# Kernel tuning notes

Hardware: AMD Instinct MI355X
Metric: run time of the kernel (lower is better)

Reference implementation:

```python
import jax, jax.numpy as jnp
import numpy as np

ND_WEIGHT = 1.0
NUM_CLASS = 1000
B, D = 16384, 2048


def setup_inputs() -> dict:
    key = jax.random.key(0)
    k1, k2, k3, k4 = jax.random.split(key, 4)
    s_emb = jax.random.normal(k1, (B, D), dtype=jnp.float32)
    t_emb = jax.random.normal(k2, (B, D), dtype=jnp.float32)
    T_EMB = jax.random.normal(k3, (NUM_CLASS, D), dtype=jnp.float32)
    labels = jax.random.randint(k4, (B,), 0, NUM_CLASS, dtype=jnp.int64)
    return {"s_emb": s_emb, "t_emb": t_emb, "T_EMB": T_EMB, "labels": labels}


def reference(s_emb, t_emb, T_EMB, labels):
    # Gather per-sample class centers: [B, D]
    centers = T_EMB[labels]
    # Unit-normalize each center (L2 along feature dim)
    e_c = centers / jnp.linalg.norm(centers, axis=-1, keepdims=True)
    # Per-sample max of student/teacher embedding norms: [B]
    s_norm = jnp.linalg.norm(s_emb, axis=-1)
    t_norm = jnp.linalg.norm(t_emb, axis=-1)
    max_norm = jnp.maximum(s_norm, t_norm)
    # 1 - <s, e_c> / max_norm, summed then averaged, scaled by nd_weight
    dots = jnp.sum(s_emb * e_c, axis=-1)
    loss_sum = jnp.sum(1.0 - dots / max_norm)
    return loss_sum * ND_WEIGHT / s_emb.shape[0]
```

## Files before the change

### kernel.cpp

```cpp
#include <hip/hip_runtime.h>


#define NROWS  16384
#define DDIM   2048
#define BLK    256
#define WPB    (BLK / 64)
#define RPW    4
#define GRID   (NROWS / (WPB * RPW))
#define GRID_AT (NROWS / WPB)

typedef float v4f __attribute__((ext_vector_type(4)));

__device__ __forceinline__ float dot4(const v4f a, const v4f b) {
    return a.x*b.x + a.y*b.y + a.z*b.z + a.w*b.w;
}

__global__ __launch_bounds__(BLK, 1) void dnl_main_kernel(
    const float* __restrict__ s_emb,
    const float* __restrict__ t_emb,
    const float* __restrict__ T_EMB,
    const int*   __restrict__ labels,
    float*       __restrict__ partial)
{
    const int tid  = threadIdx.x;
    const int lane = tid & 63;
    const int wave = blockIdx.x * WPB + (tid >> 6);
    const int row0 = wave * RPW;

    v4f sA[8], tA[8], cA[8];
    v4f sB[8], tB[8], cB[8];

    auto issue = [&](int row, v4f* S, v4f* T, v4f* C) {
        const int label = labels[row];
        const v4f* s4 = (const v4f*)(s_emb + (size_t)row   * DDIM);
        const v4f* t4 = (const v4f*)(t_emb + (size_t)row   * DDIM);
        const v4f* c4 = (const v4f*)(T_EMB + (size_t)label * DDIM);
        #pragma unroll
        for (int j = 0; j < 8; ++j) {
            const int k = lane + j * 64;
            S[j] = s4[k];
            T[j] = t4[k];
            C[j] = c4[k];
        }
    };

    auto consume = [&](int row, const v4f* S, const v4f* T, const v4f* C) {
        float ss = 0.f, tt = 0.f, sc = 0.f, cc = 0.f;
        #pragma unroll
        for (int j = 0; j < 8; ++j) {
            ss += dot4(S[j], S[j]);
            tt += dot4(T[j], T[j]);
            sc += dot4(S[j], C[j]);
            cc += dot4(C[j], C[j]);
        }
        #pragma unroll
        for (int off = 32; off > 0; off >>= 1) {
            ss += __shfl_xor(ss, off, 64);
            tt += __shfl_xor(tt, off, 64);
            sc += __shfl_xor(sc, off, 64);
            cc += __shfl_xor(cc, off, 64);
        }
        if (lane == 0) {
            const float max_norm = fmaxf(sqrtf(ss), sqrtf(tt));
            partial[row] = 1.0f - sc / (sqrtf(cc) * max_norm);
        }
    };

    issue  (row0 + 0, sA, tA, cA);
    issue  (row0 + 1, sB, tB, cB);
    consume(row0 + 0, sA, tA, cA);
    issue  (row0 + 2, sA, tA, cA);
    consume(row0 + 1, sB, tB, cB);
    issue  (row0 + 3, sB, tB, cB);
    consume(row0 + 2, sA, tA, cA);
    consume(row0 + 3, sB, tB, cB);
}

__global__ __launch_bounds__(BLK) void dnl_reduce_kernel(
    const float* __restrict__ partial,
    float*       __restrict__ out)
{
    const int tid = threadIdx.x;
    const float4* p4 = (const float4*)partial;
    float sum = 0.f;
    #pragma unroll
    for (int j = 0; j < 16; ++j) {
        const float4 v = p4[tid + j * BLK];
        sum += v.x + v.y + v.z + v.w;
    }

    #pragma unroll
    for (int off = 32; off > 0; off >>= 1)
        sum += __shfl_xor(sum, off, 64);

    __shared__ float red[4];
    if ((tid & 63) == 0) red[tid >> 6] = sum;
    __syncthreads();
    if (tid == 0)
        out[0] = (red[0] + red[1] + red[2] + red[3]) * (1.0f / (float)NROWS);
}

__global__ __launch_bounds__(BLK, 2) void dnl_main_atomic_kernel(
    const float* __restrict__ s_emb,
    const float* __restrict__ t_emb,
    const float* __restrict__ T_EMB,
    const int*   __restrict__ labels,
    float*       __restrict__ out)
{
    const int tid  = threadIdx.x;
    const int lane = tid & 63;
    const int row  = blockIdx.x * WPB + (tid >> 6);
    const int label = labels[row];

    const v4f* s4 = (const v4f*)(s_emb + (size_t)row   * DDIM);
    const v4f* t4 = (const v4f*)(t_emb + (size_t)row   * DDIM);
    const v4f* c4 = (const v4f*)(T_EMB + (size_t)label * DDIM);

    float ss = 0.f, tt = 0.f, sc = 0.f, cc = 0.f;
    #pragma unroll
    for (int j = 0; j < 8; ++j) {
        const int k = lane + j * 64;
        const v4f s = s4[k];
        const v4f t = t4[k];
        const v4f c = c4[k];
        ss += dot4(s, s);
        tt += dot4(t, t);
        sc += dot4(s, c);
        cc += dot4(c, c);
    }
    #pragma unroll
    for (int off = 32; off > 0; off >>= 1) {
        ss += __shfl_xor(ss, off, 64);
        tt += __shfl_xor(tt, off, 64);
        sc += __shfl_xor(sc, off, 64);
        cc += __shfl_xor(cc, off, 64);
    }
    if (lane == 0) {
        const float max_norm = fmaxf(sqrtf(ss), sqrtf(tt));
        atomicAdd(out, (1.0f - sc / (sqrtf(cc) * max_norm)) * (1.0f / (float)NROWS));
    }
}

extern "C" void kernel_launch(void* const* d_in, const int* in_sizes, int n_in,
                              void* d_out, int out_size, void* d_ws, size_t ws_size,
                              hipStream_t stream) {
    const float* s_emb  = (const float*)d_in[0];
    const float* t_emb  = (const float*)d_in[1];
    const float* T_EMB  = (const float*)d_in[2];
    const int*   labels = (const int*)d_in[3];
    float* out = (float*)d_out;

    if (ws_size >= (size_t)NROWS * sizeof(float)) {
        float* partial = (float*)d_ws;
        dnl_main_kernel<<<GRID, BLK, 0, stream>>>(s_emb, t_emb, T_EMB, labels, partial);
        dnl_reduce_kernel<<<1, BLK, 0, stream>>>(partial, out);
    } else {
        hipMemsetAsync(d_out, 0, sizeof(float), stream);
        dnl_main_atomic_kernel<<<GRID_AT, BLK, 0, stream>>>(s_emb, t_emb, T_EMB, labels, out);
    }
}
```

Measured before the change: 281.8 us.

## Bucket rows by label so each block reuses one class center from LDS

Adds a single-block histogram/scan kernel that groups row indices by label, then launches one block per class. Each block loads its center into LDS once, computes its norm once, and streams only the s and t rows for that class. This removes redundant center reads and per-row center-norm work. In exchange it adds a serial one-block sort kernel, an extra launch, load imbalance across classes, and one wave per row without the previous explicit load pipelining.

Result: slower. 306.3 us (+8.7%).

```diff
diff --git a/kernel.cpp b/kernel.cpp
--- a/kernel.cpp
+++ b/kernel.cpp
@@ -3,10 +3,9 @@
 
 #define NROWS  16384
 #define DDIM   2048
+#define NLAB   1000
 #define BLK    256
 #define WPB    (BLK / 64)
-#define RPW    4
-#define GRID   (NROWS / (WPB * RPW))
 #define GRID_AT (NROWS / WPB)
 
 typedef float v4f __attribute__((ext_vector_type(4)));
@@ -15,65 +14,106 @@
     return a.x*b.x + a.y*b.y + a.z*b.z + a.w*b.w;
 }
 
-__global__ __launch_bounds__(BLK, 1) void dnl_main_kernel(
+__global__ __launch_bounds__(1024) void dnl_hist_kernel(
+    const int* __restrict__ labels,
+    int*       __restrict__ offsets,
+    int*       __restrict__ list)
+{
+    __shared__ int cnt[1024];
+    __shared__ int cur[1024];
+    const int tid = threadIdx.x;
+    cnt[tid] = 0;
+    __syncthreads();
+
+    int myl[16];
+    #pragma unroll
+    for (int j = 0; j < 16; ++j)
+        myl[j] = labels[tid + j * 1024];
+    #pragma unroll
+    for (int j = 0; j < 16; ++j)
+        atomicAdd(&cnt[myl[j]], 1);
+    __syncthreads();
+
+    const int count_mine = cnt[tid];
+    for (int off = 1; off < 1024; off <<= 1) {
+        const int v = (tid >= off) ? cnt[tid - off] : 0;
+        __syncthreads();
+        cnt[tid] += v;
+        __syncthreads();
+    }
+    const int start = cnt[tid] - count_mine;
+    cur[tid] = start;
+    if (tid <= NLAB) offsets[tid] = start;
+    __syncthreads();
+
+    #pragma unroll
+    for (int j = 0; j < 16; ++j) {
+        const int row  = tid + j * 1024;
+        const int slot = atomicAdd(&cur[myl[j]], 1);
+        list[slot] = row;
+    }
+}
+
+__global__ __launch_bounds__(BLK) void dnl_label_kernel(
     const float* __restrict__ s_emb,
     const float* __restrict__ t_emb,
     const float* __restrict__ T_EMB,
-    const int*   __restrict__ labels,
+    const int*   __restrict__ offsets,
+    const int*   __restrict__ list,
     float*       __restrict__ partial)
 {
-    const int tid  = threadIdx.x;
-    const int lane = tid & 63;
-    const int wave = blockIdx.x * WPB + (tid >> 6);
-    const int row0 = wave * RPW;
-
-    v4f sA[8], tA[8], cA[8];
-    v4f sB[8], tB[8], cB[8];
-
-    auto issue = [&](int row, v4f* S, v4f* T, v4f* C) {
-        const int label = labels[row];
-        const v4f* s4 = (const v4f*)(s_emb + (size_t)row   * DDIM);
-        const v4f* t4 = (const v4f*)(t_emb + (size_t)row   * DDIM);
-        const v4f* c4 = (const v4f*)(T_EMB + (size_t)label * DDIM);
+    const int tid   = threadIdx.x;
+    const int lane  = tid & 63;
+    const int wv    = tid >> 6;
+    const int label = blockIdx.x;
+
+    const int beg = offsets[label];
+    const int end = offsets[label + 1];
+    if (beg == end) return;
+
+    __shared__ v4f cLds[512];
+    const v4f* c4 = (const v4f*)(T_EMB + (size_t)label * DDIM);
+    cLds[tid]       = c4[tid];
+    cLds[tid + 256] = c4[tid + 256];
+    __syncthreads();
+
+    v4f c[8];
+    #pragma unroll
+    for (int j = 0; j < 8; ++j) c[j] = cLds[lane + j * 64];
+
+    float cc = 0.f;
+    #pragma unroll
+    for (int j = 0; j < 8; ++j) cc += dot4(c[j], c[j]);
+    #pragma unroll
+    for (int off = 32; off > 0; off >>= 1) cc += __shfl_xor(cc, off, 64);
+    const float cnorm = sqrtf(cc);
+
+    for (int i = beg + wv; i < end; i += WPB) {
+        const int row = list[i];
+        const v4f* s4 = (const v4f*)(s_emb + (size_t)row * DDIM);
+        const v4f* t4 = (const v4f*)(t_emb + (size_t)row * DDIM);
+
+        float ss = 0.f, tt = 0.f, sc = 0.f;
         #pragma unroll
         for (int j = 0; j < 8; ++j) {
             const int k = lane + j * 64;
-            S[j] = s4[k];
-            T[j] = t4[k];
-            C[j] = c4[k];
-        }
-    };
-
-    auto consume = [&](int row, const v4f* S, const v4f* T, const v4f* C) {
-        float ss = 0.f, tt = 0.f, sc = 0.f, cc = 0.f;
-        #pragma unroll
-        for (int j = 0; j < 8; ++j) {
-            ss += dot4(S[j], S[j]);
-            tt += dot4(T[j], T[j]);
-            sc += dot4(S[j], C[j]);
-            cc += dot4(C[j], C[j]);
+            const v4f s = s4[k];
+            const v4f t = t4[k];
+            ss += dot4(s, s);
+            tt += dot4(t, t);
+            sc += dot4(s, c[j]);
         }
         #pragma unroll
         for (int off = 32; off > 0; off >>= 1) {
             ss += __shfl_xor(ss, off, 64);
             tt += __shfl_xor(tt, off, 64);
             sc += __shfl_xor(sc, off, 64);
-            cc += __shfl_xor(cc, off, 64);
         }
         if (lane == 0) {
             const float max_norm = fmaxf(sqrtf(ss), sqrtf(tt));
-            partial[row] = 1.0f - sc / (sqrtf(cc) * max_norm);
+            partial[row] = 1.0f - sc / (cnorm * max_norm);
         }
-    };
-
-    issue  (row0 + 0, sA, tA, cA);
-    issue  (row0 + 1, sB, tB, cB);
-    consume(row0 + 0, sA, tA, cA);
-    issue  (row0 + 2, sA, tA, cA);
-    consume(row0 + 1, sB, tB, cB);
-    issue  (row0 + 3, sB, tB, cB);
-    consume(row0 + 2, sA, tA, cA);
-    consume(row0 + 3, sB, tB, cB);
+    }
 }
 
 __global__ __launch_bounds__(BLK) void dnl_reduce_kernel(
@@ -88,7 +128,6 @@
         const float4 v = p4[tid + j * BLK];
         sum += v.x + v.y + v.z + v.w;
     }
-
     #pragma unroll
     for (int off = 32; off > 0; off >>= 1)
         sum += __shfl_xor(sum, off, 64);
@@ -150,9 +189,15 @@
     const int*   labels = (const int*)d_in[3];
     float* out = (float*)d_out;
 
-    if (ws_size >= (size_t)NROWS * sizeof(float)) {
+    const size_t need = (size_t)NROWS * 4 * 2 + (size_t)(NLAB + 1) * 4;
+
+    if (ws_size >= need) {
         float* partial = (float*)d_ws;
-        dnl_main_kernel<<<GRID, BLK, 0, stream>>>(s_emb, t_emb, T_EMB, labels, partial);
+        int*   list    = (int*)((char*)d_ws + (size_t)NROWS * 4);
+        int*   offsets = (int*)((char*)d_ws + (size_t)NROWS * 8);
+        dnl_hist_kernel<<<1, 1024, 0, stream>>>(labels, offsets, list);
+        dnl_label_kernel<<<NLAB, BLK, 0, stream>>>(s_emb, t_emb, T_EMB,
+                                                   offsets, list, partial);
         dnl_reduce_kernel<<<1, BLK, 0, stream>>>(partial, out);
     } else {
         hipMemsetAsync(d_out, 0, sizeof(float), stream);
```
